# Kernel tuning notes

Hardware: AMD Instinct MI355X
Metric: run time of the kernel (lower is better)

## Reference

```python
import jax, jax.numpy as jnp
import numpy as np
from jax import lax

T = 32768
DUNITS = 1024
ATT_DIM = 512
EPROJS = 512
ACONV_CHANS = 32
ACONV_FILTS = 15  # kernel = 2*15+1 = 31


def setup_inputs() -> dict:
    key = jax.random.key(0)
    ks = jax.random.split(key, 8)
    dec_z = jax.random.normal(ks[0], (1, DUNITS), jnp.float32)
    att_prev = jax.random.uniform(ks[1], (1, T), jnp.float32)
    att_prev = att_prev / jnp.sum(att_prev, axis=1, keepdims=True)  # prob-like alignment
    pre_compute_enc_h = jax.random.normal(ks[2], (1, T, ATT_DIM), jnp.float32) * 0.1
    enc_h = jax.random.normal(ks[3], (1, T, EPROJS), jnp.float32)
    mask = jnp.zeros((1, T), jnp.float32)  # additive mask (0 = keep)
    conv_w = jax.random.normal(ks[4], (ACONV_CHANS, 1, 2 * ACONV_FILTS + 1), jnp.float32) * 0.1
    conv_b = jnp.zeros((ACONV_CHANS,), jnp.float32)
    W_att = jax.random.normal(ks[5], (ATT_DIM, ACONV_CHANS), jnp.float32) * 0.1
    W_dec = jax.random.normal(ks[6], (ATT_DIM, DUNITS), jnp.float32) * 0.03
    W_g = jax.random.normal(ks[7], (1, ATT_DIM), jnp.float32) * 0.05
    b_g = jnp.zeros((1,), jnp.float32)
    return {"dec_z": dec_z, "att_prev": att_prev, "pre_compute_enc_h": pre_compute_enc_h,
            "enc_h": enc_h, "mask": mask, "conv_w": conv_w, "conv_b": conv_b,
            "W_att": W_att, "W_dec": W_dec, "W_g": W_g, "b_g": b_g}


def reference(dec_z, att_prev, pre_compute_enc_h, enc_h, mask, conv_w, conv_b, W_att, W_dec, W_g, b_g):
    scaling = 2.0
    # location conv: att_prev [1,T] -> [1,C,T] (Conv2d with height-1 kernel == Conv1d)
    att_conv = lax.conv_general_dilated(
        att_prev[:, None, :], conv_w, window_strides=(1,),
        padding=[(ACONV_FILTS, ACONV_FILTS)],
        dimension_numbers=("NCH", "OIH", "NCH"))
    att_conv = att_conv + conv_b[None, :, None]          # [1,C,T]
    att_conv = jnp.einsum("bct,ac->bta", att_conv, W_att)  # mlp_att -> [1,T,att_dim]
    dec_z_tiled = (dec_z @ W_dec.T)[:, None, :]           # [1,1,att_dim]
    # gvec over tanh sum -> energies [1,T]
    e = jnp.einsum("bta,a->bt", jnp.tanh(pre_compute_enc_h + dec_z_tiled + att_conv), W_g[0]) + b_g[0]
    e = e + mask
    w = jax.nn.softmax(scaling * e, axis=1)               # [1,T]
    # forward-attention recurrence: shift-add-mul, then L1 normalize
    att_prev_shift = jnp.pad(att_prev, ((0, 0), (1, 0)))[:, :-1]
    w = (att_prev + att_prev_shift) * w
    w = jnp.clip(w, 1e-6, None)
    w = w / jnp.sum(w, axis=1, keepdims=True)             # L1 normalize (w > 0)
    c = jnp.sum(enc_h * w[:, :, None], axis=1)            # [1,eprojs]
    return (c, w)
```

## Files before the change

kernel.cpp:

```cpp
#include <hip/hip_runtime.h>

#define T_LEN 32768
#define ADIM  512
#define NDEC  1024
#define KTAPS 31

#define WS_BASE 0
#define WS_G    512
#define WS_SARR 16384
#define WS_BMAX 49152
#define WS_BSUM 49664
#define WS_SSUM 50176
#define WS_U    50432
#define WS_CREP 83968

typedef __attribute__((ext_vector_type(8))) short bf16x8;
typedef __attribute__((ext_vector_type(4))) float f32x4;

__device__ __forceinline__ float fast_tanh(float x) {
    float e = __expf(2.0f * x);
    return 1.0f - 2.0f * __builtin_amdgcn_rcpf(e + 1.0f);
}

__device__ __forceinline__ unsigned short f2bf(float f) {
    unsigned u = __float_as_uint(f);
    return (unsigned short)((u + 0x7FFFu + ((u >> 16) & 1u)) >> 16);
}

__global__ __launch_bounds__(256) void k0_prep(
        const float* __restrict__ dec_z, const float* __restrict__ conv_w,
        const float* __restrict__ conv_b, const float* __restrict__ W_att,
        const float* __restrict__ W_dec, float* __restrict__ ws) {
    int b = blockIdx.x, tid = threadIdx.x;
    int lane = tid & 63, wave = tid >> 6;
    if (b < 64) {
        if (b == 0 && tid == 0) ws[WS_SSUM] = 0.f;
        for (int s = 0; s < 2; ++s) {
            int a = b * 8 + wave * 2 + s;
            float sum = 0.f;
            #pragma unroll
            for (int i = 0; i < 16; ++i)
                sum += W_dec[a * NDEC + i * 64 + lane] * dec_z[i * 64 + lane];
            #pragma unroll
            for (int off = 32; off > 0; off >>= 1) sum += __shfl_xor(sum, off);
            if (lane == 0) {
                float bias = 0.f;
                #pragma unroll
                for (int c = 0; c < 32; ++c) bias += conv_b[c] * W_att[a * 32 + c];
                ws[WS_BASE + a] = sum + bias;
            }
        }
    } else {
        int k = b - 64;
        unsigned short* Gf = (unsigned short*)(ws + WS_G);
        for (int s = 0; s < 2; ++s) {
            int a = 2 * tid + s;
            float g = 0.f;
            if (k < KTAPS) {
                #pragma unroll
                for (int c = 0; c < 32; ++c)
                    g += conv_w[c * KTAPS + k] * W_att[a * 32 + c];
            }
            int at = a >> 4, col = a & 15;
            int l = col | ((k >> 3) << 4), i = k & 7;
            Gf[(at * 64 + l) * 8 + i] = f2bf(g);
        }
    }
}

__global__ __launch_bounds__(512, 4) void k1_energy(
        const float* __restrict__ att_prev, const float* __restrict__ pre,
        const float* __restrict__ mask, const float* __restrict__ W_g,
        const float* __restrict__ b_g, float* __restrict__ ws) {
    __shared__ float ap_s[96];
    __shared__ float eP[2][64];
    int tid = threadIdx.x, lane = tid & 63, wave = tid >> 6;
    int tt = wave & 3, ah = wave >> 2;
    int t0 = blockIdx.x * 64;

    if (blockIdx.x < 32) ws[WS_CREP + blockIdx.x * 512 + tid] = 0.f;

    if (tid < 96) {
        int g = t0 - 15 + tid;
        ap_s[tid] = (g >= 0 && g < T_LEN) ? att_prev[g] : 0.f;
    }
    __syncthreads();

    int row = lane & 15, g4 = lane >> 4;

    bf16x8 afrag;
    int aidx = tt * 16 + row + g4 * 8;
    #pragma unroll
    for (int i = 0; i < 8; ++i) afrag[i] = (short)f2bf(ap_s[aidx + i]);

    const unsigned short* Gf = (const unsigned short*)(ws + WS_G);
    float e_acc[4] = {0.f, 0.f, 0.f, 0.f};
    int tbase = t0 + tt * 16 + g4 * 4;

    #pragma unroll 4
    for (int p = 0; p < 16; ++p) {
        int at = ah * 16 + p;
        int ac = at * 16 + row;
        bf16x8 bfrag = *(const bf16x8*)(Gf + (size_t)(at * 64 + lane) * 8);
        float bs = ws[WS_BASE + ac];
        f32x4 c = {bs, bs, bs, bs};
        c = __builtin_amdgcn_mfma_f32_16x16x32_bf16(afrag, bfrag, c, 0, 0, 0);
        float wgv = W_g[ac];
        #pragma unroll
        for (int r = 0; r < 4; ++r) {
            float pv = pre[(size_t)(tbase + r) * ADIM + ac];
            e_acc[r] = fmaf(fast_tanh(c[r] + pv), wgv, e_acc[r]);
        }
    }

    #pragma unroll
    for (int r = 0; r < 4; ++r) {
        float s = e_acc[r];
        s += __shfl_xor(s, 1); s += __shfl_xor(s, 2);
        s += __shfl_xor(s, 4); s += __shfl_xor(s, 8);
        e_acc[r] = s;
    }
    if (row == 0) {
        #pragma unroll
        for (int r = 0; r < 4; ++r) eP[ah][tt * 16 + g4 * 4 + r] = e_acc[r];
    }
    __syncthreads();

    if (wave == 0) {
        int t = t0 + lane;
        float e = eP[0][lane] + eP[1][lane];
        float sv = 2.0f * (e + b_g[0] + mask[t]);
        ws[WS_SARR + t] = sv;
        float m = sv, z = 1.0f;
        #pragma unroll
        for (int off = 32; off > 0; off >>= 1) {
            float mo = __shfl_xor(m, off), zo = __shfl_xor(z, off);
            float mn = fmaxf(m, mo);
            z = z * __expf(m - mn) + zo * __expf(mo - mn);
            m = mn;
        }
        if (lane == 0) { ws[WS_BMAX + blockIdx.x] = m; ws[WS_BSUM + blockIdx.x] = z; }
    }
}

__global__ __launch_bounds__(512) void k3_context(
        const float* __restrict__ att_prev, const float* __restrict__ enc_h,
        float* __restrict__ ws) {
    __shared__ float wmz[16];
    __shared__ float cbuf[4 * 512];
    int tid = threadIdx.x, lane = tid & 63, wave = tid >> 6;

    float m = ws[WS_BMAX + wave * 64 + lane];
    float z = ws[WS_BSUM + wave * 64 + lane];
    #pragma unroll
    for (int off = 32; off > 0; off >>= 1) {
        float mo = __shfl_xor(m, off), zo = __shfl_xor(z, off);
        float mn = fmaxf(m, mo);
        z = z * __expf(m - mn) + zo * __expf(mo - mn);
        m = mn;
    }
    if (lane == 0) { wmz[wave] = m; wmz[8 + wave] = z; }
    __syncthreads();
    float M = wmz[0], Z = wmz[8];
    #pragma unroll
    for (int w = 1; w < 8; ++w) {
        float mn = fmaxf(M, wmz[w]);
        Z = Z * __expf(M - mn) + wmz[8 + w] * __expf(wmz[w] - mn);
        M = mn;
    }
    float invZ = 1.0f / Z;

    int t0 = blockIdx.x * 32;
    int team = tid >> 7, l = tid & 127;
    int a4 = 4 * l;
    int tbase = t0 + team * 8;
    float4 acc = make_float4(0.f, 0.f, 0.f, 0.f);
    #pragma unroll
    for (int i = 0; i < 8; ++i) {
        int t = tbase + i;
        float ap0 = att_prev[t];
        float apm = (t > 0) ? att_prev[t - 1] : 0.f;
        float u = fmaxf((ap0 + apm) * __expf(ws[WS_SARR + t] - M) * invZ, 1e-6f);
        float4 e = *(const float4*)(enc_h + (size_t)t * ADIM + a4);
        acc.x = fmaf(u, e.x, acc.x);
        acc.y = fmaf(u, e.y, acc.y);
        acc.z = fmaf(u, e.z, acc.z);
        acc.w = fmaf(u, e.w, acc.w);
    }
    if (team != 0) *(float4*)&cbuf[team * 512 + a4] = acc;

    if (tid < 32) {
        int t = t0 + tid;
        float ap0 = att_prev[t];
        float apm = (t > 0) ? att_prev[t - 1] : 0.f;
        float u = fmaxf((ap0 + apm) * __expf(ws[WS_SARR + t] - M) * invZ, 1e-6f);
        ws[WS_U + t] = u;
        float s = u;
        #pragma unroll
        for (int off = 16; off > 0; off >>= 1) s += __shfl_xor(s, off, 32);
        if (tid == 0) atomicAdd(&ws[WS_SSUM], s);
    }
    __syncthreads();
    if (team == 0) {
        float4 b1 = *(const float4*)&cbuf[1 * 512 + a4];
        float4 b2 = *(const float4*)&cbuf[2 * 512 + a4];
        float4 b3 = *(const float4*)&cbuf[3 * 512 + a4];
        float* rep = ws + WS_CREP + (blockIdx.x & 31) * 512;
        atomicAdd(&rep[a4 + 0], acc.x + b1.x + b2.x + b3.x);
        atomicAdd(&rep[a4 + 1], acc.y + b1.y + b2.y + b3.y);
        atomicAdd(&rep[a4 + 2], acc.z + b1.z + b2.z + b3.z);
        atomicAdd(&rep[a4 + 3], acc.w + b1.w + b2.w + b3.w);
    }
}

__global__ __launch_bounds__(512) void k4_final(
        const float* __restrict__ ws, float* __restrict__ out) {
    int b = blockIdx.x, tid = threadIdx.x;
    float invS = 1.0f / ws[WS_SSUM];
    if (b == 0) {
        float acc = 0.f;
        #pragma unroll
        for (int r = 0; r < 32; ++r) acc += ws[WS_CREP + r * 512 + tid];
        out[tid] = acc * invS;
    } else {
        int i = (b - 1) * 512 + tid;
        out[512 + i] = ws[WS_U + i] * invS;
    }
}

extern "C" void kernel_launch(void* const* d_in, const int* in_sizes, int n_in,
                              void* d_out, int out_size, void* d_ws, size_t ws_size,
                              hipStream_t stream) {
    const float* dec_z    = (const float*)d_in[0];
    const float* att_prev = (const float*)d_in[1];
    const float* pre      = (const float*)d_in[2];
    const float* enc_h    = (const float*)d_in[3];
    const float* mask     = (const float*)d_in[4];
    const float* conv_w   = (const float*)d_in[5];
    const float* conv_b   = (const float*)d_in[6];
    const float* W_att    = (const float*)d_in[7];
    const float* W_dec    = (const float*)d_in[8];
    const float* W_g      = (const float*)d_in[9];
    const float* b_g      = (const float*)d_in[10];
    float* out = (float*)d_out;
    float* ws  = (float*)d_ws;

    k0_prep   <<<96,   256, 0, stream>>>(dec_z, conv_w, conv_b, W_att, W_dec, ws);
    k1_energy <<<512,  512, 0, stream>>>(att_prev, pre, mask, W_g, b_g, ws);
    k3_context<<<1024, 512, 0, stream>>>(att_prev, enc_h, ws);
    k4_final  <<<65,   512, 0, stream>>>(ws, out);
}
```

Measured before the change: 186.7 us.

## Stage pre_compute_enc_h rows in LDS via async global_load_lds with smaller tiles

After: 183.3 us. No clear change (-1.8%).

```diff
diff --git a/kernel.cpp b/kernel.cpp
--- a/kernel.cpp
+++ b/kernel.cpp
@@ -9,10 +9,10 @@
 #define WS_G    512
 #define WS_SARR 16384
 #define WS_BMAX 49152
-#define WS_BSUM 49664
-#define WS_SSUM 50176
-#define WS_U    50432
-#define WS_CREP 83968
+#define WS_BSUM 51200
+#define WS_SSUM 53248
+#define WS_U    53504
+#define WS_CREP 86272
 
 typedef __attribute__((ext_vector_type(8))) short bf16x8;
 typedef __attribute__((ext_vector_type(4))) float f32x4;
@@ -68,19 +68,33 @@
     }
 }
 
-__global__ __launch_bounds__(512, 4) void k1_energy(
+__global__ __launch_bounds__(512, 6) void k1_energy(
         const float* __restrict__ att_prev, const float* __restrict__ pre,
         const float* __restrict__ mask, const float* __restrict__ W_g,
         const float* __restrict__ b_g, float* __restrict__ ws) {
-    __shared__ float ap_s[96];
-    __shared__ float eP[2][64];
+    __shared__ float pre_s[16 * ADIM];
+    __shared__ float ap_s[48];
+    __shared__ float eP[8][16];
     int tid = threadIdx.x, lane = tid & 63, wave = tid >> 6;
-    int tt = wave & 3, ah = wave >> 2;
-    int t0 = blockIdx.x * 64;
+    int t0 = blockIdx.x * 16;
 
     if (blockIdx.x < 32) ws[WS_CREP + blockIdx.x * 512 + tid] = 0.f;
 
-    if (tid < 96) {
+    {
+        const float* grow = pre + (size_t)(t0 + 2 * wave) * ADIM + lane * 4;
+        float* lrow = &pre_s[(2 * wave) * ADIM];
+        #pragma unroll
+        for (int r = 0; r < 2; ++r) {
+            #pragma unroll
+            for (int h = 0; h < 2; ++h) {
+                __builtin_amdgcn_global_load_lds(
+                    (const __attribute__((address_space(1))) void*)(grow + r * ADIM + h * 256),
+                    (__attribute__((address_space(3))) void*)(lrow + r * ADIM + h * 256),
+                    16, 0, 0);
+            }
+        }
+    }
+    if (tid < 48) {
         int g = t0 - 15 + tid;
         ap_s[tid] = (g >= 0 && g < T_LEN) ? att_prev[g] : 0.f;
     }
@@ -89,17 +103,16 @@
     int row = lane & 15, g4 = lane >> 4;
 
     bf16x8 afrag;
-    int aidx = tt * 16 + row + g4 * 8;
+    int aidx = row + g4 * 8;
     #pragma unroll
     for (int i = 0; i < 8; ++i) afrag[i] = (short)f2bf(ap_s[aidx + i]);
 
     const unsigned short* Gf = (const unsigned short*)(ws + WS_G);
     float e_acc[4] = {0.f, 0.f, 0.f, 0.f};
-    int tbase = t0 + tt * 16 + g4 * 4;
-
-    #pragma unroll 4
-    for (int p = 0; p < 16; ++p) {
-        int at = ah * 16 + p;
+
+    #pragma unroll 2
+    for (int p = 0; p < 4; ++p) {
+        int at = wave * 4 + p;
         int ac = at * 16 + row;
         bf16x8 bfrag = *(const bf16x8*)(Gf + (size_t)(at * 64 + lane) * 8);
         float bs = ws[WS_BASE + ac];
@@ -108,7 +121,7 @@
         float wgv = W_g[ac];
         #pragma unroll
         for (int r = 0; r < 4; ++r) {
-            float pv = pre[(size_t)(tbase + r) * ADIM + ac];
+            float pv = pre_s[(g4 * 4 + r) * ADIM + ac];
             e_acc[r] = fmaf(fast_tanh(c[r] + pv), wgv, e_acc[r]);
         }
     }
@@ -122,16 +135,22 @@
     }
     if (row == 0) {
         #pragma unroll
-        for (int r = 0; r < 4; ++r) eP[ah][tt * 16 + g4 * 4 + r] = e_acc[r];
+        for (int r = 0; r < 4; ++r) eP[wave][g4 * 4 + r] = e_acc[r];
     }
     __syncthreads();
 
     if (wave == 0) {
-        int t = t0 + lane;
-        float e = eP[0][lane] + eP[1][lane];
-        float sv = 2.0f * (e + b_g[0] + mask[t]);
-        ws[WS_SARR + t] = sv;
-        float m = sv, z = 1.0f;
+        float sv = -1e30f, z0 = 0.f;
+        if (lane < 16) {
+            float e = 0.f;
+            #pragma unroll
+            for (int q = 0; q < 8; ++q) e += eP[q][lane];
+            int t = t0 + lane;
+            sv = 2.0f * (e + b_g[0] + mask[t]);
+            ws[WS_SARR + t] = sv;
+            z0 = 1.0f;
+        }
+        float m = sv, z = z0;
         #pragma unroll
         for (int off = 32; off > 0; off >>= 1) {
             float mo = __shfl_xor(m, off), zo = __shfl_xor(z, off);
@@ -150,8 +169,15 @@
     __shared__ float cbuf[4 * 512];
     int tid = threadIdx.x, lane = tid & 63, wave = tid >> 6;
 
-    float m = ws[WS_BMAX + wave * 64 + lane];
-    float z = ws[WS_BSUM + wave * 64 + lane];
+    float m = -1e30f, z = 0.f;
+    int base = wave * 256 + lane;
+    #pragma unroll
+    for (int q = 0; q < 4; ++q) {
+        float mo = ws[WS_BMAX + base + q * 64], zo = ws[WS_BSUM + base + q * 64];
+        float mn = fmaxf(m, mo);
+        z = z * __expf(m - mn) + zo * __expf(mo - mn);
+        m = mn;
+    }
     #pragma unroll
     for (int off = 32; off > 0; off >>= 1) {
         float mo = __shfl_xor(m, off), zo = __shfl_xor(z, off);
@@ -246,7 +272,7 @@
     float* ws  = (float*)d_ws;
 
     k0_prep   <<<96,   256, 0, stream>>>(dec_z, conv_w, conv_b, W_att, W_dec, ws);
-    k1_energy <<<512,  512, 0, stream>>>(att_prev, pre, mask, W_g, b_g, ws);
+    k1_energy <<<2048, 512, 0, stream>>>(att_prev, pre, mask, W_g, b_g, ws);
     k3_context<<<1024, 512, 0, stream>>>(att_prev, enc_h, ws);
     k4_final  <<<65,   512, 0, stream>>>(ws, out);
 }
```
